# Performance work log

Measured on AMD Instinct MI355X. Metric: run time of the kernel, lower is better.

## Reference

```python
import jax, jax.numpy as jnp
import numpy as np

VOCAB = 10000
EMB = 100
UNITS = 64
SEQ = 80
BATCH = 4096


def lstm_scan(x, W, U, b):
    """Keras-style LSTM. x: [B,T,D]; W: [D,4U]; U: [U,4U]; b: [4U].
    Gate order i, f, g(cell), o. Returns full hidden sequence [B,T,U]."""
    B = x.shape[0]
    units = U.shape[0]
    xT = jnp.swapaxes(x, 0, 1)  # [T,B,D]

    def step(carry, xt):
        h, c = carry
        z = xt @ W + h @ U + b  # [B,4U]
        i, f, g, o = jnp.split(z, 4, axis=-1)
        c = jax.nn.sigmoid(f) * c + jax.nn.sigmoid(i) * jnp.tanh(g)
        h = jax.nn.sigmoid(o) * jnp.tanh(c)
        return (h, c), h

    init = (jnp.zeros((B, units), x.dtype), jnp.zeros((B, units), x.dtype))
    _, hs = jax.lax.scan(step, init, xT)
    return jnp.swapaxes(hs, 0, 1)  # [B,T,U]


def setup_inputs() -> dict:
    key = jax.random.key(0)
    ks = jax.random.split(key, 10)
    tokens = jax.random.randint(ks[0], (BATCH, SEQ), 0, VOCAB, dtype=jnp.int32)
    s = 0.05
    emb = jax.random.normal(ks[1], (VOCAB, EMB), jnp.float32) * s
    W1 = jax.random.normal(ks[2], (EMB, 4 * UNITS), jnp.float32) * s
    U1 = jax.random.normal(ks[3], (UNITS, 4 * UNITS), jnp.float32) * s
    b1 = jnp.zeros((4 * UNITS,), jnp.float32)
    W2 = jax.random.normal(ks[4], (UNITS, 4 * UNITS), jnp.float32) * s
    U2 = jax.random.normal(ks[5], (UNITS, 4 * UNITS), jnp.float32) * s
    b2 = jnp.zeros((4 * UNITS,), jnp.float32)
    Wd = jax.random.normal(ks[6], (UNITS, 1), jnp.float32) * s
    bd = jnp.zeros((1,), jnp.float32)
    return {"tokens": tokens, "emb": emb, "W1": W1, "U1": U1, "b1": b1,
            "W2": W2, "U2": U2, "b2": b2, "Wd": Wd, "bd": bd}


def reference(tokens, emb, W1, U1, b1, W2, U2, b2, Wd, bd):
    x = emb[tokens]                      # [B,T,EMB]
    h1 = lstm_scan(x, W1, U1, b1)        # [B,T,U] (dropout inactive at inference)
    h2 = lstm_scan(h1, W2, U2, b2)       # [B,T,U]
    hlast = h2[:, -1, :]                 # second LSTM has return_sequences=False
    logits = hlast @ Wd + bd             # [B,1]
    return jax.nn.sigmoid(logits)
```

## Files before the change

### kernel.cpp

```cpp
#include <hip/hip_runtime.h>


#define VOCAB 10000
#define EMB   100
#define SEQ   80
#define BATCH 4096
#define NGRID 256

typedef _Float16 f16;
typedef _Float16 f16x8 __attribute__((ext_vector_type(8)));
typedef _Float16 half2_t __attribute__((ext_vector_type(2)));
typedef float    f32x4 __attribute__((ext_vector_type(4)));
typedef unsigned int uint;

#define LOG2E 1.4426950408889634f
#define NSC   (-LOG2E)

__device__ __forceinline__ uint pack2(float lo, float hi) {
    return __builtin_bit_cast(uint, __builtin_amdgcn_cvt_pkrtz(lo, hi));
}
__device__ __forceinline__ f32x4 mfma16(uint4 a, uint4 b, f32x4 c) {
    return __builtin_amdgcn_mfma_f32_16x16x32_f16(
        __builtin_bit_cast(f16x8, a), __builtin_bit_cast(f16x8, b), c, 0, 0, 0);
}
__device__ __forceinline__ void barrier_lds() {
    asm volatile("s_waitcnt lgkmcnt(0)\n\ts_barrier" ::: "memory");
}
__device__ __forceinline__ float sigm_exact(float x) {
    return 1.0f / (1.0f + __expf(-x));
}

__device__ __forceinline__ float lstm_epi(float zsI, float zsF, float zsG,
                                          float zsO, float& c) {
    float A = __builtin_amdgcn_exp2f(zsI);
    float B = __builtin_amdgcn_exp2f(zsF);
    float G = __builtin_amdgcn_exp2f(-2.0f * zsG);
    float C = __builtin_amdgcn_exp2f(zsO);
    float Bp = 1.0f + B;
    float P  = (1.0f + A) * (G + 1.0f);
    float Q  = (G - 1.0f) * Bp;
    c = __builtin_fmaf(c, P, Q) * __builtin_amdgcn_rcpf(P * Bp);
    float T = __builtin_amdgcn_exp2f((2.0f * LOG2E) * c);
    return (T - 1.0f) * __builtin_amdgcn_rcpf((1.0f + C) * (T + 1.0f));
}

#define WS_E1F_OFF 0
#define WS_B1F_OFF 10240000
#define WS_B2F_OFF 10272768
#define WS_NEEDED  10338304

#define NB_GEMM 160
__global__ __launch_bounds__(256) void prep_e1(
    const float* __restrict__ emb,
    const float* __restrict__ W1, const float* __restrict__ U1,
    const float* __restrict__ b1,
    const float* __restrict__ W2, const float* __restrict__ U2,
    float* __restrict__ E1f, uint* __restrict__ B1f, uint* __restrict__ B2f) {
    if (blockIdx.x < NB_GEMM) {
        const int tid  = threadIdx.x;
        const int w    = tid >> 6;
        const int lane = tid & 63;
        const int q    = lane >> 4;
        const int li   = lane & 15;
        const int v0b  = blockIdx.x * 64;
        if (v0b >= VOCAB) return;

        uint4 bf[4][4];
#pragma unroll
        for (int nf = 0; nf < 4; ++nf) {
            const int col = w * 64 + nf * 16 + li;
#pragma unroll
            for (int kt = 0; kt < 4; ++kt) {
                const int k0 = kt * 32 + q * 8;
                uint dwv[4];
#pragma unroll
                for (int dw = 0; dw < 4; ++dw) {
                    const int k = k0 + 2 * dw;
                    float lo = (k     < EMB) ? NSC * W1[k * 256 + col]       : 0.0f;
                    float hi = (k + 1 < EMB) ? NSC * W1[(k + 1) * 256 + col] : 0.0f;
                    dwv[dw] = pack2(lo, hi);
                }
                bf[nf][kt].x = dwv[0]; bf[nf][kt].y = dwv[1];
                bf[nf][kt].z = dwv[2]; bf[nf][kt].w = dwv[3];
            }
        }
        float b1v[4];
#pragma unroll
        for (int nf = 0; nf < 4; ++nf) b1v[nf] = NSC * b1[w * 64 + nf * 16 + li];

#pragma unroll 1
        for (int mt = 0; mt < 4; ++mt) {
            const int v0 = v0b + mt * 16;
            if (v0 >= VOCAB) break;
            const int vr = v0 + li;
            const float* er = emb + (size_t)((vr < VOCAB) ? vr : (VOCAB - 1)) * EMB;

            uint4 af[4];
#pragma unroll
            for (int kt = 0; kt < 3; ++kt) {
                const int k0 = kt * 32 + q * 8;
                float4 lo4 = *(const float4*)(er + k0);
                float4 hi4 = *(const float4*)(er + k0 + 4);
                af[kt].x = pack2(lo4.x, lo4.y);
                af[kt].y = pack2(lo4.z, lo4.w);
                af[kt].z = pack2(hi4.x, hi4.y);
                af[kt].w = pack2(hi4.z, hi4.w);
            }
            if (q == 0) {
                float4 t = *(const float4*)(er + 96);
                af[3].x = pack2(t.x, t.y);
                af[3].y = pack2(t.z, t.w);
                af[3].z = 0u; af[3].w = 0u;
            } else {
                af[3].x = 0u; af[3].y = 0u; af[3].z = 0u; af[3].w = 0u;
            }

            f32x4 acc[4];
#pragma unroll
            for (int nf = 0; nf < 4; ++nf) {
                acc[nf][0] = b1v[nf]; acc[nf][1] = b1v[nf];
                acc[nf][2] = b1v[nf]; acc[nf][3] = b1v[nf];
            }
#pragma unroll
            for (int kt = 0; kt < 4; ++kt)
#pragma unroll
                for (int nf = 0; nf < 4; ++nf)
                    acc[nf] = mfma16(af[kt], bf[nf][kt], acc[nf]);

            const bool full = (v0 + 16 <= VOCAB);
#pragma unroll
            for (int nf = 0; nf < 4; ++nf) {
                const int dst = (nf * 16 + li) * 4 + w;
#pragma unroll
                for (int reg = 0; reg < 4; ++reg) {
                    const int r = v0 + q * 4 + reg;
                    if (full || r < VOCAB)
                        E1f[(size_t)r * 256 + dst] = acc[nf][reg];
                }
            }
        }
    } else {
        int idx = (blockIdx.x - NB_GEMM) * 256 + threadIdx.x;
        if (idx < 8192) {
            int dw = idx & 3, lane = (idx >> 2) & 63, kt = (idx >> 8) & 1,
                g = (idx >> 9) & 3, w = idx >> 11;
            int k   = kt * 32 + (lane >> 4) * 8 + dw * 2;
            int col = g * 64 + w * 16 + (lane & 15);
            B1f[idx] = pack2(NSC * U1[k * 256 + col], NSC * U1[(k + 1) * 256 + col]);
        }
        if (idx < 16384) {
            int dw = idx & 3, lane = (idx >> 2) & 63, kt = (idx >> 8) & 3,
                g = (idx >> 10) & 3, w = idx >> 12;
            int k   = kt * 32 + (lane >> 4) * 8 + dw * 2;
            int col = g * 64 + w * 16 + (lane & 15);
            float lo = (k < 64) ? W2[k * 256 + col] : U2[(k - 64) * 256 + col];
            float hi = (k < 63) ? W2[(k + 1) * 256 + col] : U2[(k + 1 - 64) * 256 + col];
            B2f[idx] = pack2(NSC * lo, NSC * hi);
        }
    }
}

__global__ __launch_bounds__(256, 1) void lstm_mfma(
    const int* __restrict__ tokens, const f32x4* __restrict__ E1f4,
    const uint4* __restrict__ B1f, const uint4* __restrict__ B2f,
    const float* __restrict__ b2, const float* __restrict__ Wd,
    const float* __restrict__ bd, float* __restrict__ out) {
    __shared__ uint4 AbufU[512];
    __shared__ float red[64];
    f16* Abuf = (f16*)AbufU;

    const int tid  = threadIdx.x;
    const int w    = tid >> 6;
    const int lane = tid & 63;
    const int q    = lane >> 4;
    const int li   = lane & 15;
    const int u    = w * 16 + li;
    const int row0 = blockIdx.x * 16;

    const uint4 z4 = {0u, 0u, 0u, 0u};
    AbufU[tid] = z4; AbufU[tid + 256] = z4;

    uint4 b1f[4][2], b2f[4][4];
#pragma unroll
    for (int g = 0; g < 4; ++g) {
#pragma unroll
        for (int kt = 0; kt < 2; ++kt) b1f[g][kt] = B1f[((w * 4 + g) * 2 + kt) * 64 + lane];
#pragma unroll
        for (int kt = 0; kt < 4; ++kt) b2f[g][kt] = B2f[((w * 4 + g) * 4 + kt) * 64 + lane];
    }
    float b2v[4];
#pragma unroll
    for (int g = 0; g < 4; ++g) b2v[g] = NSC * b2[g * 64 + u];
    const float wdv = Wd[u];
    const float bdv = bd[0];

    int4  tokc[4], tokn[4];
    f32x4 e1buf[2][4];
#pragma unroll
    for (int r = 0; r < 4; ++r) {
        tokc[r] = *(const int4*)(tokens + (size_t)(row0 + q * 4 + r) * SEQ);
        e1buf[0][r] = E1f4[(size_t)tokc[r].x * 64 + u];
        e1buf[1][r] = E1f4[(size_t)tokc[r].y * 64 + u];
    }

    float c1[4] = {0.f, 0.f, 0.f, 0.f}, c2[4] = {0.f, 0.f, 0.f, 0.f};
    float h2v[4] = {0.f, 0.f, 0.f, 0.f};
    uint4 a1f0 = z4, a1f1 = z4, a2f0 = z4, a2f1 = z4;

    __syncthreads();

#pragma unroll 1
    for (int t4 = 0; t4 < SEQ / 4; ++t4) {
        if (t4 < SEQ / 4 - 1) {
#pragma unroll
            for (int r = 0; r < 4; ++r)
                tokn[r] = *(const int4*)(tokens + (size_t)(row0 + q * 4 + r) * SEQ + (t4 + 1) * 4);
        }
#pragma unroll
        for (int s = 0; s < 4; ++s) {
            const int p = s & 1;
            f32x4 acc[4];
#pragma unroll
            for (int g = 0; g < 4; ++g) {
#pragma unroll
                for (int r = 0; r < 4; ++r) acc[g][r] = e1buf[p][r][g];
            }
#pragma unroll
            for (int g = 0; g < 4; ++g) acc[g] = mfma16(a1f0, b1f[g][0], acc[g]);
#pragma unroll
            for (int g = 0; g < 4; ++g) acc[g] = mfma16(a1f1, b1f[g][1], acc[g]);

            f32x4 acc2[4];
#pragma unroll
            for (int g = 0; g < 4; ++g) {
                acc2[g][0] = b2v[g]; acc2[g][1] = b2v[g];
                acc2[g][2] = b2v[g]; acc2[g][3] = b2v[g];
            }
#pragma unroll
            for (int g = 0; g < 4; ++g) acc2[g] = mfma16(a1f0, b2f[g][0], acc2[g]);
#pragma unroll
            for (int g = 0; g < 4; ++g) acc2[g] = mfma16(a1f1, b2f[g][1], acc2[g]);
#pragma unroll
            for (int g = 0; g < 4; ++g) acc2[g] = mfma16(a2f0, b2f[g][2], acc2[g]);
#pragma unroll
            for (int g = 0; g < 4; ++g) acc2[g] = mfma16(a2f1, b2f[g][3], acc2[g]);

#pragma unroll
            for (int r = 0; r < 4; ++r) {
                float h1 = lstm_epi(acc[0][r], acc[1][r], acc[2][r], acc[3][r], c1[r]);
                Abuf[p * 2048 + ((u >> 3) * 16 + 4 * q + r) * 8 + (u & 7)] = (f16)h1;
            }

            if (t4 | s) {
#pragma unroll
                for (int r = 0; r < 4; ++r) {
                    h2v[r] = lstm_epi(acc2[0][r], acc2[1][r], acc2[2][r], acc2[3][r], c2[r]);
                    Abuf[p * 2048 + 1024 + ((u >> 3) * 16 + 4 * q + r) * 8 + (u & 7)] = (f16)h2v[r];
                }
            }

            if (t4 * 4 + s + 2 < SEQ) {
#pragma unroll
                for (int r = 0; r < 4; ++r) {
                    int tk = (s == 0) ? tokc[r].z : (s == 1) ? tokc[r].w
                           : (s == 2) ? tokn[r].x : tokn[r].y;
                    e1buf[p][r] = E1f4[(size_t)tk * 64 + u];
                }
            }

            barrier_lds();

            a1f0 = AbufU[p * 256 + lane];
            a1f1 = AbufU[p * 256 + 64 + lane];
            a2f0 = AbufU[p * 256 + 128 + lane];
            a2f1 = AbufU[p * 256 + 192 + lane];
        }
#pragma unroll
        for (int r = 0; r < 4; ++r) tokc[r] = tokn[r];
    }

    {
        f32x4 acc2[4];
#pragma unroll
        for (int g = 0; g < 4; ++g) {
            acc2[g][0] = b2v[g]; acc2[g][1] = b2v[g];
            acc2[g][2] = b2v[g]; acc2[g][3] = b2v[g];
        }
#pragma unroll
        for (int g = 0; g < 4; ++g) acc2[g] = mfma16(a1f0, b2f[g][0], acc2[g]);
#pragma unroll
        for (int g = 0; g < 4; ++g) acc2[g] = mfma16(a1f1, b2f[g][1], acc2[g]);
#pragma unroll
        for (int g = 0; g < 4; ++g) acc2[g] = mfma16(a2f0, b2f[g][2], acc2[g]);
#pragma unroll
        for (int g = 0; g < 4; ++g) acc2[g] = mfma16(a2f1, b2f[g][3], acc2[g]);
#pragma unroll
        for (int r = 0; r < 4; ++r)
            h2v[r] = lstm_epi(acc2[0][r], acc2[1][r], acc2[2][r], acc2[3][r], c2[r]);
    }

#pragma unroll
    for (int r = 0; r < 4; ++r) {
        float pv = h2v[r] * wdv;
        pv += __shfl_xor(pv, 1, 64);
        pv += __shfl_xor(pv, 2, 64);
        pv += __shfl_xor(pv, 4, 64);
        pv += __shfl_xor(pv, 8, 64);
        if (li == 0) red[w * 16 + q * 4 + r] = pv;
    }
    __syncthreads();
    if (tid < 16) {
        float sum = red[tid] + red[16 + tid] + red[32 + tid] + red[48 + tid] + bdv;
        out[row0 + tid] = sigm_exact(sum);
    }
}

__device__ __forceinline__ float lane_bcast(float v, int j) {
    return __builtin_bit_cast(float, __builtin_amdgcn_readlane(__builtin_bit_cast(int, v), j));
}
__device__ __forceinline__ float sigm_f(float x)  { return 1.0f / (1.0f + __expf(-x)); }
__device__ __forceinline__ float tanh_f(float x)  { return 2.0f / (1.0f + __expf(-2.0f * x)) - 1.0f; }

__global__ __launch_bounds__(512) void lstm_fused_fallback(
    const int* __restrict__ tokens, const float* __restrict__ emb,
    const float* __restrict__ W1, const float* __restrict__ U1, const float* __restrict__ b1,
    const float* __restrict__ W2, const float* __restrict__ U2, const float* __restrict__ b2,
    const float* __restrict__ Wd, const float* __restrict__ bd, float* __restrict__ out) {
    const int lane = threadIdx.x & 63;
    const int wave = threadIdx.x >> 6;
    const int row0 = blockIdx.x * 16 + wave * 2;
    float bias1[4], bias2[4];
#pragma unroll
    for (int g = 0; g < 4; ++g) { bias1[g] = b1[g * 64 + lane]; bias2[g] = b2[g * 64 + lane]; }
    const float wd = Wd[lane]; const float bdv = bd[0];
    float h1[2] = {0.f, 0.f}, c1[2] = {0.f, 0.f}, h2[2] = {0.f, 0.f}, c2[2] = {0.f, 0.f};
#pragma unroll 1
    for (int t = 0; t < SEQ; ++t) {
        float acc[4][2];
#pragma unroll
        for (int g = 0; g < 4; ++g) { acc[g][0] = bias1[g]; acc[g][1] = bias1[g]; }
        int tokA = __builtin_amdgcn_readfirstlane(tokens[(row0 + 0) * SEQ + t]);
        int tokB = __builtin_amdgcn_readfirstlane(tokens[(row0 + 1) * SEQ + t]);
        const float4* xA = (const float4*)(emb + (size_t)tokA * EMB);
        const float4* xB = (const float4*)(emb + (size_t)tokB * EMB);
#pragma unroll 5
        for (int d4 = 0; d4 < EMB / 4; ++d4) {
            float4 a4 = xA[d4]; float4 b4 = xB[d4];
            float av[4] = {a4.x, a4.y, a4.z, a4.w}; float bv[4] = {b4.x, b4.y, b4.z, b4.w};
#pragma unroll
            for (int e = 0; e < 4; ++e) {
                const float* wrow = W1 + (d4 * 4 + e) * 256;
#pragma unroll
                for (int g = 0; g < 4; ++g) {
                    float wv = wrow[g * 64 + lane];
                    acc[g][0] += av[e] * wv; acc[g][1] += bv[e] * wv;
                }
            }
        }
#pragma unroll 4
        for (int j = 0; j < 64; ++j) {
            float ha = lane_bcast(h1[0], j), hb = lane_bcast(h1[1], j);
            const float* urow = U1 + j * 256;
#pragma unroll
            for (int g = 0; g < 4; ++g) {
                float wv = urow[g * 64 + lane];
                acc[g][0] += ha * wv; acc[g][1] += hb * wv;
            }
        }
#pragma unroll
        for (int r = 0; r < 2; ++r) {
            float ig = sigm_f(acc[0][r]), fg = sigm_f(acc[1][r]);
            float gg = tanh_f(acc[2][r]), og = sigm_f(acc[3][r]);
            c1[r] = fg * c1[r] + ig * gg; h1[r] = og * tanh_f(c1[r]);
        }
        float acc2[4][2];
#pragma unroll
        for (int g = 0; g < 4; ++g) { acc2[g][0] = bias2[g]; acc2[g][1] = bias2[g]; }
#pragma unroll 4
        for (int j = 0; j < 64; ++j) {
            float pa = lane_bcast(h1[0], j), pb = lane_bcast(h1[1], j);
            float qa = lane_bcast(h2[0], j), qb = lane_bcast(h2[1], j);
            const float* w2row = W2 + j * 256; const float* u2row = U2 + j * 256;
#pragma unroll
            for (int g = 0; g < 4; ++g) {
                float w2v = w2row[g * 64 + lane], u2v = u2row[g * 64 + lane];
                acc2[g][0] += pa * w2v + qa * u2v;
                acc2[g][1] += pb * w2v + qb * u2v;
            }
        }
#pragma unroll
        for (int r = 0; r < 2; ++r) {
            float ig = sigm_f(acc2[0][r]), fg = sigm_f(acc2[1][r]);
            float gg = tanh_f(acc2[2][r]), og = sigm_f(acc2[3][r]);
            c2[r] = fg * c2[r] + ig * gg; h2[r] = og * tanh_f(c2[r]);
        }
    }
#pragma unroll
    for (int r = 0; r < 2; ++r) {
        float p = h2[r] * wd;
#pragma unroll
        for (int off = 32; off > 0; off >>= 1) p += __shfl_down(p, off, 64);
        if (lane == 0) out[row0 + r] = sigm_f(p + bdv);
    }
}

extern "C" void kernel_launch(void* const* d_in, const int* in_sizes, int n_in,
                              void* d_out, int out_size, void* d_ws, size_t ws_size,
                              hipStream_t stream) {
    const int*   tokens = (const int*)  d_in[0];
    const float* emb    = (const float*)d_in[1];
    const float* W1     = (const float*)d_in[2];
    const float* U1     = (const float*)d_in[3];
    const float* b1     = (const float*)d_in[4];
    const float* W2     = (const float*)d_in[5];
    const float* U2     = (const float*)d_in[6];
    const float* b2     = (const float*)d_in[7];
    const float* Wd     = (const float*)d_in[8];
    const float* bd     = (const float*)d_in[9];
    float* out = (float*)d_out;

    if (ws_size < (size_t)WS_NEEDED) {
        lstm_fused_fallback<<<256, 512, 0, stream>>>(tokens, emb, W1, U1, b1, W2, U2, b2, Wd, bd, out);
        return;
    }

    char*  ws  = (char*)d_ws;
    float* E1f = (float*)(ws + WS_E1F_OFF);
    uint*  B1f = (uint*) (ws + WS_B1F_OFF);
    uint*  B2f = (uint*) (ws + WS_B2F_OFF);

    prep_e1  <<<NB_GEMM + 64, 256, 0, stream>>>(emb, W1, U1, b1, W2, U2, E1f, B1f, B2f);
    lstm_mfma<<<NGRID, 256, 0, stream>>>(tokens, (const f32x4*)E1f,
                                         (const uint4*)B1f, (const uint4*)B2f,
                                         b2, Wd, bd, out);
}
```

Baseline: 166.1 us.

## Interleave layer-2 MFMAs with layer-1 epilogue and fold tanh scaling into weights

Measured after the change: 165.8 us. Within noise of the previous version (-0.2%).

```diff
diff --git a/kernel.cpp b/kernel.cpp
--- a/kernel.cpp
+++ b/kernel.cpp
@@ -15,6 +15,7 @@
 
 #define LOG2E 1.4426950408889634f
 #define NSC   (-LOG2E)
+#define GSC   (2.0f * LOG2E)
 
 __device__ __forceinline__ uint pack2(float lo, float hi) {
     return __builtin_bit_cast(uint, __builtin_amdgcn_cvt_pkrtz(lo, hi));
@@ -25,6 +26,10 @@
 }
 __device__ __forceinline__ void barrier_lds() {
     asm volatile("s_waitcnt lgkmcnt(0)\n\ts_barrier" ::: "memory");
+}
+template <int MASK, int N>
+__device__ __forceinline__ void sgb() {
+    __builtin_amdgcn_sched_group_barrier(MASK, N, 0);
 }
 __device__ __forceinline__ float sigm_exact(float x) {
     return 1.0f / (1.0f + __expf(-x));
@@ -34,7 +39,7 @@
                                           float zsO, float& c) {
     float A = __builtin_amdgcn_exp2f(zsI);
     float B = __builtin_amdgcn_exp2f(zsF);
-    float G = __builtin_amdgcn_exp2f(-2.0f * zsG);
+    float G = __builtin_amdgcn_exp2f(zsG);
     float C = __builtin_amdgcn_exp2f(zsO);
     float Bp = 1.0f + B;
     float P  = (1.0f + A) * (G + 1.0f);
@@ -65,6 +70,8 @@
         const int v0b  = blockIdx.x * 64;
         if (v0b >= VOCAB) return;
 
+        const float sc = (w == 2) ? GSC : NSC;
+
         uint4 bf[4][4];
 #pragma unroll
         for (int nf = 0; nf < 4; ++nf) {
@@ -76,8 +83,8 @@
 #pragma unroll
                 for (int dw = 0; dw < 4; ++dw) {
                     const int k = k0 + 2 * dw;
-                    float lo = (k     < EMB) ? NSC * W1[k * 256 + col]       : 0.0f;
-                    float hi = (k + 1 < EMB) ? NSC * W1[(k + 1) * 256 + col] : 0.0f;
+                    float lo = (k     < EMB) ? sc * W1[k * 256 + col]       : 0.0f;
+                    float hi = (k + 1 < EMB) ? sc * W1[(k + 1) * 256 + col] : 0.0f;
                     dwv[dw] = pack2(lo, hi);
                 }
                 bf[nf][kt].x = dwv[0]; bf[nf][kt].y = dwv[1];
@@ -86,7 +93,7 @@
         }
         float b1v[4];
 #pragma unroll
-        for (int nf = 0; nf < 4; ++nf) b1v[nf] = NSC * b1[w * 64 + nf * 16 + li];
+        for (int nf = 0; nf < 4; ++nf) b1v[nf] = sc * b1[w * 64 + nf * 16 + li];
 
 #pragma unroll 1
         for (int mt = 0; mt < 4; ++mt) {
@@ -146,16 +153,18 @@
                 g = (idx >> 9) & 3, w = idx >> 11;
             int k   = kt * 32 + (lane >> 4) * 8 + dw * 2;
             int col = g * 64 + w * 16 + (lane & 15);
-            B1f[idx] = pack2(NSC * U1[k * 256 + col], NSC * U1[(k + 1) * 256 + col]);
+            float sc = (g == 2) ? GSC : NSC;
+            B1f[idx] = pack2(sc * U1[k * 256 + col], sc * U1[(k + 1) * 256 + col]);
         }
         if (idx < 16384) {
             int dw = idx & 3, lane = (idx >> 2) & 63, kt = (idx >> 8) & 3,
                 g = (idx >> 10) & 3, w = idx >> 12;
             int k   = kt * 32 + (lane >> 4) * 8 + dw * 2;
             int col = g * 64 + w * 16 + (lane & 15);
+            float sc = (g == 2) ? GSC : NSC;
             float lo = (k < 64) ? W2[k * 256 + col] : U2[(k - 64) * 256 + col];
             float hi = (k < 63) ? W2[(k + 1) * 256 + col] : U2[(k + 1 - 64) * 256 + col];
-            B2f[idx] = pack2(NSC * lo, NSC * hi);
+            B2f[idx] = pack2(sc * lo, sc * hi);
         }
     }
 }
@@ -190,7 +199,8 @@
     }
     float b2v[4];
 #pragma unroll
-    for (int g = 0; g < 4; ++g) b2v[g] = NSC * b2[g * 64 + u];
+    for (int g = 0; g < 4; ++g)
+        b2v[g] = ((g == 2) ? GSC : NSC) * b2[g * 64 + u];
     const float wdv = Wd[u];
     const float bdv = bd[0];
 
@@ -219,7 +229,8 @@
 #pragma unroll
         for (int s = 0; s < 4; ++s) {
             const int p = s & 1;
-            f32x4 acc[4];
+
+            f32x4 acc[4], acc2[4];
 #pragma unroll
             for (int g = 0; g < 4; ++g) {
 #pragma unroll
@@ -227,28 +238,22 @@
             }
 #pragma unroll
             for (int g = 0; g < 4; ++g) acc[g] = mfma16(a1f0, b1f[g][0], acc[g]);
-#pragma unroll
-            for (int g = 0; g < 4; ++g) acc[g] = mfma16(a1f1, b1f[g][1], acc[g]);
-
-            f32x4 acc2[4];
 #pragma unroll
             for (int g = 0; g < 4; ++g) {
                 acc2[g][0] = b2v[g]; acc2[g][1] = b2v[g];
                 acc2[g][2] = b2v[g]; acc2[g][3] = b2v[g];
             }
 #pragma unroll
-            for (int g = 0; g < 4; ++g) acc2[g] = mfma16(a1f0, b2f[g][0], acc2[g]);
-#pragma unroll
-            for (int g = 0; g < 4; ++g) acc2[g] = mfma16(a1f1, b2f[g][1], acc2[g]);
-#pragma unroll
-            for (int g = 0; g < 4; ++g) acc2[g] = mfma16(a2f0, b2f[g][2], acc2[g]);
-#pragma unroll
-            for (int g = 0; g < 4; ++g) acc2[g] = mfma16(a2f1, b2f[g][3], acc2[g]);
-
-#pragma unroll
-            for (int r = 0; r < 4; ++r) {
-                float h1 = lstm_epi(acc[0][r], acc[1][r], acc[2][r], acc[3][r], c1[r]);
-                Abuf[p * 2048 + ((u >> 3) * 16 + 4 * q + r) * 8 + (u & 7)] = (f16)h1;
+            for (int g = 0; g < 4; ++g) acc[g] = mfma16(a1f1, b1f[g][1], acc[g]);
+
+#pragma unroll
+            for (int kt = 0; kt < 4; ++kt) {
+                const uint4 af = (kt == 0) ? a1f0 : (kt == 1) ? a1f1
+                               : (kt == 2) ? a2f0 : a2f1;
+#pragma unroll
+                for (int g = 0; g < 4; ++g) acc2[g] = mfma16(af, b2f[g][kt], acc2[g]);
+                float h1 = lstm_epi(acc[0][kt], acc[1][kt], acc[2][kt], acc[3][kt], c1[kt]);
+                Abuf[p * 2048 + ((u >> 3) * 16 + 4 * q + kt) * 8 + (u & 7)] = (f16)h1;
             }
 
             if (t4 | s) {
@@ -267,6 +272,13 @@
                     e1buf[p][r] = E1f4[(size_t)tk * 64 + u];
                 }
             }
+
+            sgb<0x2, 16>(); sgb<0x8, 4>();
+            sgb<0x2, 16>(); sgb<0x8, 4>();
+            sgb<0x8, 4>(); sgb<0x2, 40>();
+            sgb<0x8, 4>(); sgb<0x2, 40>();
+            sgb<0x8, 4>(); sgb<0x2, 40>();
+            sgb<0x8, 4>(); sgb<0x2, 40>();
 
             barrier_lds();
 
```

## Split LSTM layers across separate wave groups and fold tanh scale into weights

Applied to the files above, without the earlier changes.

Measured after the change: 149.5 us, median of 2. 1.11x faster.

```diff
diff --git a/kernel.cpp b/kernel.cpp
--- a/kernel.cpp
+++ b/kernel.cpp
@@ -15,6 +15,7 @@
 
 #define LOG2E 1.4426950408889634f
 #define NSC   (-LOG2E)
+#define GSC   (2.0f * LOG2E)
 
 __device__ __forceinline__ uint pack2(float lo, float hi) {
     return __builtin_bit_cast(uint, __builtin_amdgcn_cvt_pkrtz(lo, hi));
@@ -34,7 +35,7 @@
                                           float zsO, float& c) {
     float A = __builtin_amdgcn_exp2f(zsI);
     float B = __builtin_amdgcn_exp2f(zsF);
-    float G = __builtin_amdgcn_exp2f(-2.0f * zsG);
+    float G = __builtin_amdgcn_exp2f(zsG);
     float C = __builtin_amdgcn_exp2f(zsO);
     float Bp = 1.0f + B;
     float P  = (1.0f + A) * (G + 1.0f);
@@ -65,6 +66,8 @@
         const int v0b  = blockIdx.x * 64;
         if (v0b >= VOCAB) return;
 
+        const float sc = (w == 2) ? GSC : NSC;
+
         uint4 bf[4][4];
 #pragma unroll
         for (int nf = 0; nf < 4; ++nf) {
@@ -76,8 +79,8 @@
 #pragma unroll
                 for (int dw = 0; dw < 4; ++dw) {
                     const int k = k0 + 2 * dw;
-                    float lo = (k     < EMB) ? NSC * W1[k * 256 + col]       : 0.0f;
-                    float hi = (k + 1 < EMB) ? NSC * W1[(k + 1) * 256 + col] : 0.0f;
+                    float lo = (k     < EMB) ? sc * W1[k * 256 + col]       : 0.0f;
+                    float hi = (k + 1 < EMB) ? sc * W1[(k + 1) * 256 + col] : 0.0f;
                     dwv[dw] = pack2(lo, hi);
                 }
                 bf[nf][kt].x = dwv[0]; bf[nf][kt].y = dwv[1];
@@ -86,7 +89,7 @@
         }
         float b1v[4];
 #pragma unroll
-        for (int nf = 0; nf < 4; ++nf) b1v[nf] = NSC * b1[w * 64 + nf * 16 + li];
+        for (int nf = 0; nf < 4; ++nf) b1v[nf] = sc * b1[w * 64 + nf * 16 + li];
 
 #pragma unroll 1
         for (int mt = 0; mt < 4; ++mt) {
@@ -146,21 +149,23 @@
                 g = (idx >> 9) & 3, w = idx >> 11;
             int k   = kt * 32 + (lane >> 4) * 8 + dw * 2;
             int col = g * 64 + w * 16 + (lane & 15);
-            B1f[idx] = pack2(NSC * U1[k * 256 + col], NSC * U1[(k + 1) * 256 + col]);
+            float sc = (g == 2) ? GSC : NSC;
+            B1f[idx] = pack2(sc * U1[k * 256 + col], sc * U1[(k + 1) * 256 + col]);
         }
         if (idx < 16384) {
             int dw = idx & 3, lane = (idx >> 2) & 63, kt = (idx >> 8) & 3,
                 g = (idx >> 10) & 3, w = idx >> 12;
             int k   = kt * 32 + (lane >> 4) * 8 + dw * 2;
             int col = g * 64 + w * 16 + (lane & 15);
+            float sc = (g == 2) ? GSC : NSC;
             float lo = (k < 64) ? W2[k * 256 + col] : U2[(k - 64) * 256 + col];
             float hi = (k < 63) ? W2[(k + 1) * 256 + col] : U2[(k + 1 - 64) * 256 + col];
-            B2f[idx] = pack2(NSC * lo, NSC * hi);
-        }
-    }
-}
-
-__global__ __launch_bounds__(256, 1) void lstm_mfma(
+            B2f[idx] = pack2(sc * lo, sc * hi);
+        }
+    }
+}
+
+__global__ __launch_bounds__(512, 1) void lstm_mfma(
     const int* __restrict__ tokens, const f32x4* __restrict__ E1f4,
     const uint4* __restrict__ B1f, const uint4* __restrict__ B2f,
     const float* __restrict__ b2, const float* __restrict__ Wd,
@@ -171,47 +176,60 @@
 
     const int tid  = threadIdx.x;
     const int w    = tid >> 6;
+    const bool isL1 = (w < 4);
+    const int wl   = w & 3;
     const int lane = tid & 63;
     const int q    = lane >> 4;
     const int li   = lane & 15;
-    const int u    = w * 16 + li;
+    const int u    = wl * 16 + li;
     const int row0 = blockIdx.x * 16;
 
     const uint4 z4 = {0u, 0u, 0u, 0u};
-    AbufU[tid] = z4; AbufU[tid + 256] = z4;
-
-    uint4 b1f[4][2], b2f[4][4];
-#pragma unroll
-    for (int g = 0; g < 4; ++g) {
-#pragma unroll
-        for (int kt = 0; kt < 2; ++kt) b1f[g][kt] = B1f[((w * 4 + g) * 2 + kt) * 64 + lane];
-#pragma unroll
-        for (int kt = 0; kt < 4; ++kt) b2f[g][kt] = B2f[((w * 4 + g) * 4 + kt) * 64 + lane];
-    }
-    float b2v[4];
-#pragma unroll
-    for (int g = 0; g < 4; ++g) b2v[g] = NSC * b2[g * 64 + u];
-    const float wdv = Wd[u];
+    AbufU[tid] = z4;
+
     const float bdv = bd[0];
 
+    uint4 b1f[4][2];
     int4  tokc[4], tokn[4];
     f32x4 e1buf[2][4];
-#pragma unroll
-    for (int r = 0; r < 4; ++r) {
-        tokc[r] = *(const int4*)(tokens + (size_t)(row0 + q * 4 + r) * SEQ);
-        e1buf[0][r] = E1f4[(size_t)tokc[r].x * 64 + u];
-        e1buf[1][r] = E1f4[(size_t)tokc[r].y * 64 + u];
-    }
-
-    float c1[4] = {0.f, 0.f, 0.f, 0.f}, c2[4] = {0.f, 0.f, 0.f, 0.f};
+    float c1[4] = {0.f, 0.f, 0.f, 0.f};
+    uint4 b2f[4][4];
+    float b2v[4];
+    float c2[4] = {0.f, 0.f, 0.f, 0.f};
     float h2v[4] = {0.f, 0.f, 0.f, 0.f};
+    float wdv = 0.f;
+
+    if (isL1) {
+#pragma unroll
+        for (int g = 0; g < 4; ++g)
+#pragma unroll
+            for (int kt = 0; kt < 2; ++kt)
+                b1f[g][kt] = B1f[((wl * 4 + g) * 2 + kt) * 64 + lane];
+#pragma unroll
+        for (int r = 0; r < 4; ++r) {
+            tokc[r] = *(const int4*)(tokens + (size_t)(row0 + q * 4 + r) * SEQ);
+            e1buf[0][r] = E1f4[(size_t)tokc[r].x * 64 + u];
+            e1buf[1][r] = E1f4[(size_t)tokc[r].y * 64 + u];
+        }
+    } else {
+#pragma unroll
+        for (int g = 0; g < 4; ++g)
+#pragma unroll
+            for (int kt = 0; kt < 4; ++kt)
+                b2f[g][kt] = B2f[((wl * 4 + g) * 4 + kt) * 64 + lane];
+#pragma unroll
+        for (int g = 0; g < 4; ++g)
+            b2v[g] = ((g == 2) ? GSC : NSC) * b2[g * 64 + u];
+        wdv = Wd[u];
+    }
+
     uint4 a1f0 = z4, a1f1 = z4, a2f0 = z4, a2f1 = z4;
 
     __syncthreads();
 
 #pragma unroll 1
     for (int t4 = 0; t4 < SEQ / 4; ++t4) {
-        if (t4 < SEQ / 4 - 1) {
+        if (isL1 && t4 < SEQ / 4 - 1) {
 #pragma unroll
             for (int r = 0; r < 4; ++r)
                 tokn[r] = *(const int4*)(tokens + (size_t)(row0 + q * 4 + r) * SEQ + (t4 + 1) * 4);
@@ -219,52 +237,55 @@
 #pragma unroll
         for (int s = 0; s < 4; ++s) {
             const int p = s & 1;
-            f32x4 acc[4];
-#pragma unroll
-            for (int g = 0; g < 4; ++g) {
-#pragma unroll
-                for (int r = 0; r < 4; ++r) acc[g][r] = e1buf[p][r][g];
-            }
-#pragma unroll
-            for (int g = 0; g < 4; ++g) acc[g] = mfma16(a1f0, b1f[g][0], acc[g]);
-#pragma unroll
-            for (int g = 0; g < 4; ++g) acc[g] = mfma16(a1f1, b1f[g][1], acc[g]);
-
-            f32x4 acc2[4];
-#pragma unroll
-            for (int g = 0; g < 4; ++g) {
-                acc2[g][0] = b2v[g]; acc2[g][1] = b2v[g];
-                acc2[g][2] = b2v[g]; acc2[g][3] = b2v[g];
-            }
-#pragma unroll
-            for (int g = 0; g < 4; ++g) acc2[g] = mfma16(a1f0, b2f[g][0], acc2[g]);
-#pragma unroll
-            for (int g = 0; g < 4; ++g) acc2[g] = mfma16(a1f1, b2f[g][1], acc2[g]);
-#pragma unroll
-            for (int g = 0; g < 4; ++g) acc2[g] = mfma16(a2f0, b2f[g][2], acc2[g]);
-#pragma unroll
-            for (int g = 0; g < 4; ++g) acc2[g] = mfma16(a2f1, b2f[g][3], acc2[g]);
-
-#pragma unroll
-            for (int r = 0; r < 4; ++r) {
-                float h1 = lstm_epi(acc[0][r], acc[1][r], acc[2][r], acc[3][r], c1[r]);
-                Abuf[p * 2048 + ((u >> 3) * 16 + 4 * q + r) * 8 + (u & 7)] = (f16)h1;
-            }
-
-            if (t4 | s) {
+
+            if (isL1) {
+                f32x4 acc[4];
+#pragma unroll
+                for (int g = 0; g < 4; ++g) {
+#pragma unroll
+                    for (int r = 0; r < 4; ++r) acc[g][r] = e1buf[p][r][g];
+                }
+#pragma unroll
+                for (int g = 0; g < 4; ++g) acc[g] = mfma16(a1f0, b1f[g][0], acc[g]);
+#pragma unroll
+                for (int g = 0; g < 4; ++g) acc[g] = mfma16(a1f1, b1f[g][1], acc[g]);
+
 #pragma unroll
                 for (int r = 0; r < 4; ++r) {
-                    h2v[r] = lstm_epi(acc2[0][r], acc2[1][r], acc2[2][r], acc2[3][r], c2[r]);
-                    Abuf[p * 2048 + 1024 + ((u >> 3) * 16 + 4 * q + r) * 8 + (u & 7)] = (f16)h2v[r];
-                }
-            }
-
-            if (t4 * 4 + s + 2 < SEQ) {
-#pragma unroll
-                for (int r = 0; r < 4; ++r) {
-                    int tk = (s == 0) ? tokc[r].z : (s == 1) ? tokc[r].w
-                           : (s == 2) ? tokn[r].x : tokn[r].y;
-                    e1buf[p][r] = E1f4[(size_t)tk * 64 + u];
+                    float h1 = lstm_epi(acc[0][r], acc[1][r], acc[2][r], acc[3][r], c1[r]);
+                    Abuf[p * 2048 + ((u >> 3) * 16 + 4 * q + r) * 8 + (u & 7)] = (f16)h1;
+                }
+
+                if (t4 * 4 + s + 2 < SEQ) {
+#pragma unroll
+                    for (int r = 0; r < 4; ++r) {
+                        int tk = (s == 0) ? tokc[r].z : (s == 1) ? tokc[r].w
+                               : (s == 2) ? tokn[r].x : tokn[r].y;
+                        e1buf[p][r] = E1f4[(size_t)tk * 64 + u];
+                    }
+                }
+            } else {
+                f32x4 acc2[4];
+#pragma unroll
+                for (int g = 0; g < 4; ++g) {
+                    acc2[g][0] = b2v[g]; acc2[g][1] = b2v[g];
+                    acc2[g][2] = b2v[g]; acc2[g][3] = b2v[g];
+                }
+#pragma unroll
+                for (int g = 0; g < 4; ++g) acc2[g] = mfma16(a1f0, b2f[g][0], acc2[g]);
+#pragma unroll
+                for (int g = 0; g < 4; ++g) acc2[g] = mfma16(a1f1, b2f[g][1], acc2[g]);
+#pragma unroll
+                for (int g = 0; g < 4; ++g) acc2[g] = mfma16(a2f0, b2f[g][2], acc2[g]);
+#pragma unroll
+                for (int g = 0; g < 4; ++g) acc2[g] = mfma16(a2f1, b2f[g][3], acc2[g]);
+
+                if (t4 | s) {
+#pragma unroll
+                    for (int r = 0; r < 4; ++r) {
+                        h2v[r] = lstm_epi(acc2[0][r], acc2[1][r], acc2[2][r], acc2[3][r], c2[r]);
+                        Abuf[p * 2048 + 1024 + ((u >> 3) * 16 + 4 * q + r) * 8 + (u & 7)] = (f16)h2v[r];
+                    }
                 }
             }
 
@@ -272,14 +293,18 @@
 
             a1f0 = AbufU[p * 256 + lane];
             a1f1 = AbufU[p * 256 + 64 + lane];
-            a2f0 = AbufU[p * 256 + 128 + lane];
-            a2f1 = AbufU[p * 256 + 192 + lane];
-        }
-#pragma unroll
-        for (int r = 0; r < 4; ++r) tokc[r] = tokn[r];
-    }
-
-    {
+            if (!isL1) {
+                a2f0 = AbufU[p * 256 + 128 + lane];
+                a2f1 = AbufU[p * 256 + 192 + lane];
+            }
+        }
+        if (isL1) {
+#pragma unroll
+            for (int r = 0; r < 4; ++r) tokc[r] = tokn[r];
+        }
+    }
+
+    if (!isL1) {
         f32x4 acc2[4];
 #pragma unroll
         for (int g = 0; g < 4; ++g) {
@@ -297,16 +322,16 @@
 #pragma unroll
         for (int r = 0; r < 4; ++r)
             h2v[r] = lstm_epi(acc2[0][r], acc2[1][r], acc2[2][r], acc2[3][r], c2[r]);
-    }
-
-#pragma unroll
-    for (int r = 0; r < 4; ++r) {
-        float pv = h2v[r] * wdv;
-        pv += __shfl_xor(pv, 1, 64);
-        pv += __shfl_xor(pv, 2, 64);
-        pv += __shfl_xor(pv, 4, 64);
-        pv += __shfl_xor(pv, 8, 64);
-        if (li == 0) red[w * 16 + q * 4 + r] = pv;
+
+#pragma unroll
+        for (int r = 0; r < 4; ++r) {
+            float pv = h2v[r] * wdv;
+            pv += __shfl_xor(pv, 1, 64);
+            pv += __shfl_xor(pv, 2, 64);
+            pv += __shfl_xor(pv, 4, 64);
+            pv += __shfl_xor(pv, 8, 64);
+            if (li == 0) red[wl * 16 + q * 4 + r] = pv;
+        }
     }
     __syncthreads();
     if (tid < 16) {
@@ -430,7 +455,7 @@
     uint*  B2f = (uint*) (ws + WS_B2F_OFF);
 
     prep_e1  <<<NB_GEMM + 64, 256, 0, stream>>>(emb, W1, U1, b1, W2, U2, E1f, B1f, B2f);
-    lstm_mfma<<<NGRID, 256, 0, stream>>>(tokens, (const f32x4*)E1f,
+    lstm_mfma<<<NGRID, 512, 0, stream>>>(tokens, (const f32x4*)E1f,
                                          (const uint4*)B1f, (const uint4*)B2f,
                                          b2, Wd, bd, out);
 }
```
